# Kernel optimization log

Hardware: AMD Instinct MI355X
Metric: run time of the kernel (lower is better)

## Reference

```python
import jax, jax.numpy as jnp
import numpy as np

NUM_LAYERS = 32
IN_SIZE = 1024
OUT_SIZE = 1024
B, S = 32, 256


def setup_inputs() -> dict:
    key = jax.random.key(0)
    k1, k2, k3 = jax.random.split(key, 3)
    x = jax.random.normal(k1, (B, S, IN_SIZE), dtype=jnp.float32)
    layer_idx = jax.random.randint(k2, (S,), 0, NUM_LAYERS, dtype=jnp.int32)
    # learned parameter: per-layer weight [L, O, D], normal(stddev=1.0) as in flax init
    weight = jax.random.normal(k3, (NUM_LAYERS, OUT_SIZE, IN_SIZE), dtype=jnp.float32)
    return {"x": x, "layer_idx": layer_idx, "weight": weight}


def reference(x, layer_idx, weight):
    # x: [B, S, D]; layer_idx: [S]; weight: [L, O, D]
    # Each sequence position s uses expert weight[layer_idx[s]]:
    #   out[b, s, o] = sum_d x[b, s, d] * weight[layer_idx[s], o, d]
    w = weight[layer_idx]                      # [S, O, D] gather
    return jnp.einsum('bsd,sod->bso', x, w)    # [B, S, O]
```

## Files before the change

### kernel.cpp

```cpp
#include <hip/hip_runtime.h>
#include <hip/hip_bf16.h>
#include <stdint.h>

#define NLAYERS 32
#define DSIZE   1024
#define OSIZE   1024
#define BATCH   32
#define SEQ     256

#define WS_PERM  16
#define WS_TILE  512
#define MAX_TILES 88

typedef __attribute__((ext_vector_type(8)))  short short8;
typedef __attribute__((ext_vector_type(16))) float f32x16;

#define LDSTRIDE 72
#define BK 64

__global__ void prep_kernel(const int* __restrict__ layer_idx, int* __restrict__ wsi) {
    __shared__ int cnt[NLAYERS];
    __shared__ int start_[NLAYERS];
    __shared__ int cursor[NLAYERS];
    const int t = threadIdx.x;
    if (t < NLAYERS) cnt[t] = 0;
    __syncthreads();
    int l = 0;
    if (t < SEQ) { l = layer_idx[t]; atomicAdd(&cnt[l], 1); }
    __syncthreads();
    if (t == 0) {
        int acc = 0;
        for (int i = 0; i < NLAYERS; ++i) { start_[i] = acc; cursor[i] = acc; acc += cnt[i]; }
    }
    __syncthreads();
    if (t < SEQ) {
        int r = atomicAdd(&cursor[l], 1);
        wsi[WS_PERM + r] = t;
    }
    if (t == 0) {
        int nt = 0;
        for (int i = 0; i < NLAYERS; ++i) {
            const int c = cnt[i];
            for (int j = 0; j < c; j += 4) {
                wsi[WS_TILE + nt*4 + 0] = i;
                wsi[WS_TILE + nt*4 + 1] = start_[i] + j;
                wsi[WS_TILE + nt*4 + 2] = (c - j < 4) ? (c - j) : 4;
                ++nt;
            }
        }
        wsi[0] = nt;
    }
}

static __device__ __forceinline__ unsigned pk2(float a, float b) {
    unsigned ua = __builtin_bit_cast(unsigned, a) + 0x8000u;
    unsigned ub = __builtin_bit_cast(unsigned, b) + 0x8000u;
    return __builtin_amdgcn_perm(ub, ua, 0x07060302u);
}

__global__ __launch_bounds__(256, 2) void gemm_kernel(
        const float* __restrict__ x, const float* __restrict__ wgt,
        const int* __restrict__ wsi, float* __restrict__ out) {
    const int ntiles = wsi[0];
    const int mt = blockIdx.y;
    if (mt >= ntiles) return;
    const int layer     = wsi[WS_TILE + mt*4 + 0];
    const int rank_base = wsi[WS_TILE + mt*4 + 1];
    const int nranks    = wsi[WS_TILE + mt*4 + 2];
    const int ntile     = blockIdx.x;

    __shared__ __align__(16) short ldsA[128 * LDSTRIDE];
    __shared__ __align__(16) short ldsB[128 * LDSTRIDE];

    const int t     = threadIdx.x;
    const int c4    = (t & 15) * 4;
    const int rbase = t >> 4;

    int svals[2];
    bool svalid[4];
    int sv[4];
    #pragma unroll
    for (int j = 0; j < 4; ++j) {
        svalid[j] = (j < nranks);
        sv[j] = svalid[j] ? wsi[WS_PERM + rank_base + j] : 0;
    }
    (void)svals;

    const float* aptr[8];
    #pragma unroll
    for (int p = 0; p < 8; ++p) {
        const int roff = p >> 1;
        const int b    = rbase + ((p & 1) << 4);
        aptr[p] = x + (((size_t)(b * SEQ + sv[roff])) << 10) + c4;
    }
    const float* bbase = wgt + (((size_t)((layer << 10) + ntile * 128 + rbase)) << 10) + c4;

    float4 ra[8], rb[8];
    auto load_step = [&](int kk) {
        #pragma unroll
        for (int p = 0; p < 8; ++p) {
            if (svalid[p >> 1]) ra[p] = *(const float4*)(aptr[p] + kk);
            else                ra[p] = make_float4(0.f, 0.f, 0.f, 0.f);
            rb[p] = *(const float4*)(bbase + ((size_t)p << 14) + kk);
        }
    };

    const int lane = t & 63;
    const int wv   = t >> 6;
    const int wm   = (wv & 1) * 64;
    const int wn   = (wv >> 1) * 64;
    const int l31  = lane & 31;
    const int lh   = lane >> 5;

    f32x16 acc[2][2];
    #pragma unroll
    for (int mi = 0; mi < 2; ++mi)
        #pragma unroll
        for (int ni = 0; ni < 2; ++ni)
            #pragma unroll
            for (int r = 0; r < 16; ++r) acc[mi][ni][r] = 0.f;

    const short* pA0 = &ldsA[(wm + l31) * LDSTRIDE + lh * 8];
    const short* pB0 = &ldsB[(wn + l31) * LDSTRIDE + lh * 8];

    load_step(0);
    #pragma unroll 1
    for (int kk = 0; kk < DSIZE; kk += BK) {
        __syncthreads();
        #pragma unroll
        for (int p = 0; p < 8; ++p) {
            const int row = rbase + 16 * p;
            uint2 va, vb;
            va.x = pk2(ra[p].x, ra[p].y);
            va.y = pk2(ra[p].z, ra[p].w);
            vb.x = pk2(rb[p].x, rb[p].y);
            vb.y = pk2(rb[p].z, rb[p].w);
            *(uint2*)&ldsA[row * LDSTRIDE + c4] = va;
            *(uint2*)&ldsB[row * LDSTRIDE + c4] = vb;
        }
        __syncthreads();
        if (kk + BK < DSIZE) load_step(kk + BK);
        #pragma unroll
        for (int sub = 0; sub < 4; ++sub) {
            short8 a0 = *(const short8*)(pA0 + sub*16);
            short8 a1 = *(const short8*)(pA0 + 32*LDSTRIDE + sub*16);
            short8 b0 = *(const short8*)(pB0 + sub*16);
            short8 b1 = *(const short8*)(pB0 + 32*LDSTRIDE + sub*16);
            acc[0][0] = __builtin_amdgcn_mfma_f32_32x32x16_bf16(a0, b0, acc[0][0], 0, 0, 0);
            acc[0][1] = __builtin_amdgcn_mfma_f32_32x32x16_bf16(a0, b1, acc[0][1], 0, 0, 0);
            acc[1][0] = __builtin_amdgcn_mfma_f32_32x32x16_bf16(a1, b0, acc[1][0], 0, 0, 0);
            acc[1][1] = __builtin_amdgcn_mfma_f32_32x32x16_bf16(a1, b1, acc[1][1], 0, 0, 0);
        }
    }

    #pragma unroll
    for (int mi = 0; mi < 2; ++mi) {
        const int roff = (wv & 1) * 2 + mi;
        if (roff >= nranks) continue;
        const int s = wsi[WS_PERM + rank_base + roff];
        #pragma unroll
        for (int ni = 0; ni < 2; ++ni) {
            const int ocol = ntile * 128 + wn + ni * 32 + l31;
            #pragma unroll
            for (int r = 0; r < 16; ++r) {
                const int brow = (r & 3) + 8 * (r >> 2) + 4 * lh;
                out[(((size_t)(brow * SEQ + s)) << 10) + ocol] = acc[mi][ni][r];
            }
        }
    }
}

extern "C" void kernel_launch(void* const* d_in, const int* in_sizes, int n_in,
                              void* d_out, int out_size, void* d_ws, size_t ws_size,
                              hipStream_t stream) {
    const float* x         = (const float*)d_in[0];
    const int*   layer_idx = (const int*)  d_in[1];
    const float* weight    = (const float*)d_in[2];
    float* out = (float*)d_out;
    int*   wsi = (int*)d_ws;

    prep_kernel<<<1, 256, 0, stream>>>(layer_idx, wsi);
    gemm_kernel<<<dim3(8, MAX_TILES), 256, 0, stream>>>(x, weight, wsi, out);
}
```

Measured before the change: 259.8 us.

## Pre-convert activations to bf16 in a separate pass and raise occupancy target

Adds a conversion kernel that casts all of x to bf16 into workspace, so the GEMM loads half as many bytes for the A operand and skips the per-tile pack work. Each x row is otherwise re-read and re-converted by all 8 N-tile blocks. The GEMM is templated with a fallback fp32 path used when the workspace is too small, and launch bounds go from 2 to 4 blocks per CU. The extra pass reads 32 MB and writes 16 MB per call, and the higher occupancy target may force register spills.

After: 304.7 us. 1.17x slower.

```diff
diff --git a/kernel.cpp b/kernel.cpp
--- a/kernel.cpp
+++ b/kernel.cpp
@@ -11,6 +11,7 @@
 #define WS_PERM  16
 #define WS_TILE  512
 #define MAX_TILES 88
+#define XBF_OFF  65536
 
 typedef __attribute__((ext_vector_type(8)))  short short8;
 typedef __attribute__((ext_vector_type(16))) float f32x16;
@@ -58,9 +59,26 @@
     return __builtin_amdgcn_perm(ub, ua, 0x07060302u);
 }
 
-__global__ __launch_bounds__(256, 2) void gemm_kernel(
-        const float* __restrict__ x, const float* __restrict__ wgt,
-        const int* __restrict__ wsi, float* __restrict__ out) {
+__global__ __launch_bounds__(256) void xconv_kernel(const float4* __restrict__ x4,
+                                                    uint2* __restrict__ xb) {
+    const int tid = blockIdx.x * 256 + threadIdx.x;
+    const int NT  = 1024 * 256;
+    #pragma unroll
+    for (int i = 0; i < 8; ++i) {
+        const int idx = tid + i * NT;
+        float4 v = x4[idx];
+        uint2 o;
+        o.x = pk2(v.x, v.y);
+        o.y = pk2(v.z, v.w);
+        xb[idx] = o;
+    }
+}
+
+template<bool PREBF>
+__global__ __launch_bounds__(256, 4) void gemm_kernel(
+        const float* __restrict__ x, const unsigned short* __restrict__ xbf,
+        const float* __restrict__ wgt, const int* __restrict__ wsi,
+        float* __restrict__ out) {
     const int ntiles = wsi[0];
     const int mt = blockIdx.y;
     if (mt >= ntiles) return;
@@ -72,37 +90,54 @@
     __shared__ __align__(16) short ldsA[128 * LDSTRIDE];
     __shared__ __align__(16) short ldsB[128 * LDSTRIDE];
 
-    const int t     = threadIdx.x;
-    const int c4    = (t & 15) * 4;
-    const int rbase = t >> 4;
-
-    int svals[2];
+    const int t = threadIdx.x;
+
     bool svalid[4];
-    int sv[4];
+    int  sv[4];
     #pragma unroll
     for (int j = 0; j < 4; ++j) {
         svalid[j] = (j < nranks);
         sv[j] = svalid[j] ? wsi[WS_PERM + rank_base + j] : 0;
     }
-    (void)svals;
-
-    const float* aptr[8];
+
+    const int c4     = (t & 15) * 4;
+    const int rbaseB = t >> 4;
+    const float* bbase = wgt + (((size_t)((layer << 10) + ntile * 128 + rbaseB)) << 10) + c4;
+
+    const int c8      = (t & 7) * 8;
+    const int rbaseA8 = t >> 3;
+    const unsigned short* aptr8[4];
+    #pragma unroll
+    for (int p = 0; p < 4; ++p)
+        aptr8[p] = xbf + (((size_t)(rbaseA8 * SEQ + sv[p])) << 10) + c8;
+    const int rbaseA4 = t >> 4;
+    const float* aptr4[8];
     #pragma unroll
     for (int p = 0; p < 8; ++p) {
-        const int roff = p >> 1;
-        const int b    = rbase + ((p & 1) << 4);
-        aptr[p] = x + (((size_t)(b * SEQ + sv[roff])) << 10) + c4;
-    }
-    const float* bbase = wgt + (((size_t)((layer << 10) + ntile * 128 + rbase)) << 10) + c4;
-
-    float4 ra[8], rb[8];
+        const int b = rbaseA4 + ((p & 1) << 4);
+        aptr4[p] = x + (((size_t)(b * SEQ + sv[p >> 1])) << 10) + c4;
+    }
+
+    short8 ra16[4];
+    float4 ra32[8];
+    float4 rb[8];
     auto load_step = [&](int kk) {
-        #pragma unroll
-        for (int p = 0; p < 8; ++p) {
-            if (svalid[p >> 1]) ra[p] = *(const float4*)(aptr[p] + kk);
-            else                ra[p] = make_float4(0.f, 0.f, 0.f, 0.f);
-            rb[p] = *(const float4*)(bbase + ((size_t)p << 14) + kk);
-        }
+        if (PREBF) {
+            #pragma unroll
+            for (int p = 0; p < 4; ++p) {
+                if (svalid[p]) ra16[p] = *(const short8*)(aptr8[p] + kk);
+                else           ra16[p] = short8{0,0,0,0,0,0,0,0};
+            }
+        } else {
+            #pragma unroll
+            for (int p = 0; p < 8; ++p) {
+                if (svalid[p >> 1]) ra32[p] = *(const float4*)(aptr4[p] + kk);
+                else                ra32[p] = make_float4(0.f, 0.f, 0.f, 0.f);
+            }
+        }
+        #pragma unroll
+        for (int p = 0; p < 8; ++p)
+            rb[p] = *(const float4*)(bbase + ((size_t)(16 * p) << 10) + kk);
     };
 
     const int lane = t & 63;
@@ -127,15 +162,28 @@
     #pragma unroll 1
     for (int kk = 0; kk < DSIZE; kk += BK) {
         __syncthreads();
+        if (PREBF) {
+            #pragma unroll
+            for (int p = 0; p < 4; ++p) {
+                const int row = rbaseA8 + 32 * p;
+                *(short8*)&ldsA[row * LDSTRIDE + c8] = ra16[p];
+            }
+        } else {
+            #pragma unroll
+            for (int p = 0; p < 8; ++p) {
+                const int row = rbaseA4 + 16 * p;
+                uint2 va;
+                va.x = pk2(ra32[p].x, ra32[p].y);
+                va.y = pk2(ra32[p].z, ra32[p].w);
+                *(uint2*)&ldsA[row * LDSTRIDE + c4] = va;
+            }
+        }
         #pragma unroll
         for (int p = 0; p < 8; ++p) {
-            const int row = rbase + 16 * p;
-            uint2 va, vb;
-            va.x = pk2(ra[p].x, ra[p].y);
-            va.y = pk2(ra[p].z, ra[p].w);
+            const int row = rbaseB + 16 * p;
+            uint2 vb;
             vb.x = pk2(rb[p].x, rb[p].y);
             vb.y = pk2(rb[p].z, rb[p].w);
-            *(uint2*)&ldsA[row * LDSTRIDE + c4] = va;
             *(uint2*)&ldsB[row * LDSTRIDE + c4] = vb;
         }
         __syncthreads();
@@ -157,7 +205,7 @@
     for (int mi = 0; mi < 2; ++mi) {
         const int roff = (wv & 1) * 2 + mi;
         if (roff >= nranks) continue;
-        const int s = wsi[WS_PERM + rank_base + roff];
+        const int s = sv[roff];
         #pragma unroll
         for (int ni = 0; ni < 2; ++ni) {
             const int ocol = ntile * 128 + wn + ni * 32 + l31;
@@ -178,7 +226,15 @@
     const float* weight    = (const float*)d_in[2];
     float* out = (float*)d_out;
     int*   wsi = (int*)d_ws;
-
+    unsigned short* xbf = (unsigned short*)((char*)d_ws + XBF_OFF);
+
+    const bool prebf = ws_size >= (size_t)XBF_OFF + ((size_t)1 << 24);
+
+    if (prebf)
+        xconv_kernel<<<1024, 256, 0, stream>>>((const float4*)x, (uint2*)xbf);
     prep_kernel<<<1, 256, 0, stream>>>(layer_idx, wsi);
-    gemm_kernel<<<dim3(8, MAX_TILES), 256, 0, stream>>>(x, weight, wsi, out);
-}
+    if (prebf)
+        gemm_kernel<true ><<<dim3(8, MAX_TILES), 256, 0, stream>>>(x, xbf, weight, wsi, out);
+    else
+        gemm_kernel<false><<<dim3(8, MAX_TILES), 256, 0, stream>>>(x, xbf, weight, wsi, out);
+}
```
